# Optimization experiments

Measured on AMD Instinct MI355X. Metric: run time of the kernel, lower is better.

The kernel has to match this reference:

```python
import jax, jax.numpy as jnp
import numpy as np

PROBES = ["Fp1", "F3", "C3", "P3", "F7", "T3", "T5", "O1", "Fz", "Cz", "Pz",
          "Fp2", "F4", "C4", "P4", "F8", "T4", "T6", "O2"]
PROBE2IDX = {p: i for i, p in enumerate(PROBES)}
PROBE_GROUPS = {
    "LL": ["Fp1", "F7", "T3", "T5", "O1"],
    "LP": ["Fp1", "F3", "C3", "P3", "O1"],
    "RP": ["Fp2", "F8", "T4", "T6", "O2"],
    "RL": ["Fp2", "F4", "C4", "P4", "O2"],
    "Z": ["Fz", "Cz", "Pz"],
}
# Precompute bipolar-montage gather indices (18 derived channels)
_p1, _p2 = [], []
for _, probes in PROBE_GROUPS.items():
    for a, b in zip(probes[:-1], probes[1:]):
        _p1.append(PROBE2IDX[a]); _p2.append(PROBE2IDX[b])
I1 = np.asarray(_p1, dtype=np.int32)
I2 = np.asarray(_p2, dtype=np.int32)

FS = 200.0
FC_HP = 0.5
FC_LP = 50.0
Q = 0.7071067811865476  # torchaudio default Q = 1/sqrt(2)


def _biquad_coeffs(fs, fc, highpass):
    # torchaudio.functional.highpass_biquad / lowpass_biquad coefficients
    w0 = 2.0 * np.pi * fc / fs
    alpha = np.sin(w0) / (2.0 * Q)
    cw = np.cos(w0)
    a0 = 1.0 + alpha
    if highpass:
        b0 = (1.0 + cw) / 2.0
        b1 = -(1.0 + cw)
    else:
        b0 = (1.0 - cw) / 2.0
        b1 = 1.0 - cw
    b2 = b0
    a1 = -2.0 * cw
    a2 = 1.0 - alpha
    return (np.float32(b0 / a0), np.float32(b1 / a0), np.float32(b2 / a0),
            np.float32(a1 / a0), np.float32(a2 / a0))


def _biquad(x, coeffs):
    """Direct-form-I biquad along the last (time) axis. x: (B, C, T)."""
    b0, b1, b2, a1, a2 = coeffs

    def step(carry, xn):
        x1, x2, y1, y2 = carry
        y = b0 * xn + b1 * x1 + b2 * x2 - a1 * y1 - a2 * y2
        return (xn, x1, y, y1), y

    xt = jnp.moveaxis(x, -1, 0)  # (T, B, C)
    z = jnp.zeros_like(xt[0])
    _, yt = jax.lax.scan(step, (z, z, z, z), xt)
    return jnp.moveaxis(yt, 0, -1)  # (B, C, T)


def setup_inputs() -> dict:
    key = jax.random.key(0)
    k1, _ = jax.random.split(key)
    B, T, C = 64, 16384, 19
    x = jax.random.normal(k1, (B, T, C), dtype=jnp.float32)
    mask = jnp.ones((B, T, C), dtype=jnp.float32)
    return {"x": x, "mask": mask}


def reference(x, mask):
    # Bipolar montage: gather probe pairs and difference. (B, T, 18)
    d = x[..., I1] - x[..., I2]
    m = mask[..., I1] * mask[..., I2]
    eeg = jnp.swapaxes(d * m, 1, 2)       # apply_mask=True -> (B, 18, T)
    eeg_mask = jnp.swapaxes(m, 1, 2)      # (B, 18, T)
    # Cascaded biquad IIR: highpass(0.5 Hz) then lowpass(50 Hz)
    eeg = _biquad(eeg, _biquad_coeffs(FS, FC_HP, highpass=True))
    eeg = _biquad(eeg, _biquad_coeffs(FS, FC_LP, highpass=False))
    # clip_val is None -> no clamp
    return eeg, eeg_mask
```

## Files before the change

kernel.cpp:

```cpp
#include <hip/hip_runtime.h>
#include <cmath>

#define B_SZ 64
#define T_LEN 16384
#define NCH 18
#define NPROBE 19
#define TT 256
#define NTILE (T_LEN / TT)

typedef float nfloat4 __attribute__((ext_vector_type(4)));
typedef _Float16 half8 __attribute__((ext_vector_type(8)));

struct FiltConsts {
  float b0, b1, b2, a1, a2;
  float m[8][4];
};
struct BothFilt { FiltConsts f[2]; };

__device__ __forceinline__ int sw_idx(int idx) {
  return (idx & ~63) | ((idx + (idx >> 6)) & 63);
}

template <bool HALF_WS>
__global__ __launch_bounds__(256)
void montage_kernel(const float* __restrict__ x, const float* __restrict__ mask,
                    float* __restrict__ out, _Float16* __restrict__ wh) {
  __shared__ float buf[TT * NPROBE];
  const int tid = threadIdx.x;
  const int b = blockIdx.x >> 6;
  const int tile = blockIdx.x & 63;
  const int t0 = tile * TT;

  const size_t gbase = ((size_t)b * T_LEN + t0) * NPROBE;
  constexpr int N4 = TT * NPROBE / 4;

  const float4* xg = reinterpret_cast<const float4*>(x + gbase);
#pragma unroll
  for (int k = 0; k < 5; ++k) {
    int i = tid + k * 256;
    if (i < N4) reinterpret_cast<float4*>(buf)[i] = xg[i];
  }
  __syncthreads();
  float xv[NPROBE];
#pragma unroll
  for (int j = 0; j < NPROBE; ++j) xv[j] = buf[tid * NPROBE + j];
  __syncthreads();

  const float4* mg = reinterpret_cast<const float4*>(mask + gbase);
#pragma unroll
  for (int k = 0; k < 5; ++k) {
    int i = tid + k * 256;
    if (i < N4) reinterpret_cast<float4*>(buf)[i] = mg[i];
  }
  __syncthreads();
  float mv[NPROBE];
#pragma unroll
  for (int j = 0; j < NPROBE; ++j) mv[j] = buf[tid * NPROBE + j];

  const int I1[NCH] = {0,4,5,6, 0,1,2,3, 11,15,16,17, 11,12,13,14, 8,9};
  const int I2[NCH] = {4,5,6,7, 1,2,3,7, 15,16,17,18, 12,13,14,18, 9,10};
  const int t = t0 + tid;
  const size_t base = (size_t)b * NCH * T_LEN + t;
  const size_t half = (size_t)B_SZ * NCH * T_LEN;
#pragma unroll
  for (int ch = 0; ch < NCH; ++ch) {
    float d = xv[I1[ch]] - xv[I2[ch]];
    float m = mv[I1[ch]] * mv[I2[ch]];
    if (HALF_WS) {
      wh[base + (size_t)ch * T_LEN] = (_Float16)(d * m);
    } else {
      out[base + (size_t)ch * T_LEN] = d * m;
    }
    __builtin_nontemporal_store(m, &out[half + base + (size_t)ch * T_LEN]);
  }
}

template <bool HALF_WS>
__global__ __launch_bounds__(256)
void filter_kernel(float* __restrict__ out, const _Float16* __restrict__ wh,
                   BothFilt fc) {
  __shared__ float row[T_LEN];
  __shared__ float2 scanbuf[256];
  const int tid = threadIdx.x;
  float* rp = out + (size_t)blockIdx.x * T_LEN;

  if (HALF_WS) {
    const half8* hp = reinterpret_cast<const half8*>(wh + (size_t)blockIdx.x * T_LEN);
#pragma unroll
    for (int k = 0; k < 8; ++k) {
      int i8 = tid + k * 256;
      half8 v = hp[i8];
      int e = i8 * 8;
#pragma unroll
      for (int j = 0; j < 8; ++j) row[sw_idx(e + j)] = (float)v[j];
    }
  } else {
#pragma unroll
    for (int k = 0; k < 16; ++k) {
      int i4 = tid + k * 256;
      float4 v = reinterpret_cast<const float4*>(rp)[i4];
      int e = i4 * 4;
      row[sw_idx(e + 0)] = v.x; row[sw_idx(e + 1)] = v.y;
      row[sw_idx(e + 2)] = v.z; row[sw_idx(e + 3)] = v.w;
    }
  }
  __syncthreads();

  const int e0 = tid * 64;
#pragma unroll
  for (int f = 0; f < 2; ++f) {
    const FiltConsts& F = fc.f[f];
    const float b0 = F.b0, b1 = F.b1, b2 = F.b2;
    const float na1 = -F.a1, na2 = -F.a2;

    float x1 = 0.f, x2 = 0.f;
    if (tid > 0) { x1 = row[sw_idx(e0 - 1)]; x2 = row[sw_idx(e0 - 2)]; }
    __syncthreads();
    float y1 = 0.f, y2 = 0.f;
#pragma unroll 4
    for (int n = 0; n < 64; ++n) {
      int a = sw_idx(e0 + n);
      float xn = row[a];
      float acc = b0 * xn;
      acc = fmaf(b1, x1, acc);
      acc = fmaf(b2, x2, acc);
      acc = fmaf(na1, y1, acc);
      acc = fmaf(na2, y2, acc);
      row[a] = acc;
      x2 = x1; x1 = xn;
      y2 = y1; y1 = acc;
    }
    scanbuf[tid] = make_float2(y1, y2);
    __syncthreads();

#pragma unroll
    for (int k = 0; k < 8; ++k) {
      const int off = 1 << k;
      const bool act = (tid >= off);
      float2 prev, mine;
      if (act) { prev = scanbuf[tid - off]; mine = scanbuf[tid]; }
      __syncthreads();
      if (act) {
        scanbuf[tid] = make_float2(
            fmaf(F.m[k][0], prev.x, fmaf(F.m[k][1], prev.y, mine.x)),
            fmaf(F.m[k][2], prev.x, fmaf(F.m[k][3], prev.y, mine.y)));
      }
      __syncthreads();
    }

    if (tid > 0) {
      float2 s = scanbuf[tid - 1];
      float c1 = s.x, c2 = s.y;
#pragma unroll 4
      for (int n = 0; n < 64; ++n) {
        int a = sw_idx(e0 + n);
        float cn = fmaf(na1, c1, na2 * c2);
        row[a] += cn;
        c2 = c1; c1 = cn;
      }
    }
    __syncthreads();
  }

#pragma unroll
  for (int k = 0; k < 16; ++k) {
    int i4 = tid + k * 256;
    int e = i4 * 4;
    nfloat4 v = { row[sw_idx(e + 0)], row[sw_idx(e + 1)],
                  row[sw_idx(e + 2)], row[sw_idx(e + 3)] };
    __builtin_nontemporal_store(v, reinterpret_cast<nfloat4*>(rp) + i4);
  }
}

static inline void mat2mul(const double* A, const double* Bm, double* C) {
  double c0 = A[0]*Bm[0] + A[1]*Bm[2];
  double c1 = A[0]*Bm[1] + A[1]*Bm[3];
  double c2 = A[2]*Bm[0] + A[3]*Bm[2];
  double c3 = A[2]*Bm[1] + A[3]*Bm[3];
  C[0]=c0; C[1]=c1; C[2]=c2; C[3]=c3;
}

static void fill_filt(FiltConsts* F, double fc, bool hp) {
  const double Q = 0.7071067811865476;
  const double fs = 200.0;
  const double PI = 3.14159265358979323846;
  double w0 = 2.0 * PI * fc / fs;
  double alpha = std::sin(w0) / (2.0 * Q);
  double cw = std::cos(w0);
  double a0 = 1.0 + alpha;
  double b0, b1;
  if (hp) { b0 = (1.0 + cw) * 0.5; b1 = -(1.0 + cw); }
  else    { b0 = (1.0 - cw) * 0.5; b1 = (1.0 - cw); }
  double b2 = b0;
  double a1 = -2.0 * cw;
  double a2 = 1.0 - alpha;
  F->b0 = (float)(b0 / a0); F->b1 = (float)(b1 / a0); F->b2 = (float)(b2 / a0);
  F->a1 = (float)(a1 / a0); F->a2 = (float)(a2 / a0);
  double A[4] = { -(double)F->a1, -(double)F->a2, 1.0, 0.0 };
  double M[4] = { A[0], A[1], A[2], A[3] };
  for (int i = 0; i < 6; ++i) mat2mul(M, M, M);
  for (int k = 0; k < 8; ++k) {
    F->m[k][0] = (float)M[0]; F->m[k][1] = (float)M[1];
    F->m[k][2] = (float)M[2]; F->m[k][3] = (float)M[3];
    mat2mul(M, M, M);
  }
}

extern "C" void kernel_launch(void* const* d_in, const int* in_sizes, int n_in,
                              void* d_out, int out_size, void* d_ws, size_t ws_size,
                              hipStream_t stream) {
  const float* x    = (const float*)d_in[0];
  const float* mask = (const float*)d_in[1];
  float* out = (float*)d_out;
  _Float16* wh = (_Float16*)d_ws;

  BothFilt bf;
  fill_filt(&bf.f[0], 0.5, true);
  fill_filt(&bf.f[1], 50.0, false);

  const size_t ws_needed = (size_t)B_SZ * NCH * T_LEN * sizeof(_Float16);
  if (ws_size >= ws_needed) {
    hipLaunchKernelGGL((montage_kernel<true>), dim3(B_SZ * NTILE), dim3(256), 0, stream,
                       x, mask, out, wh);
    hipLaunchKernelGGL((filter_kernel<true>), dim3(B_SZ * NCH), dim3(256), 0, stream,
                       out, wh, bf);
  } else {
    hipLaunchKernelGGL((montage_kernel<false>), dim3(B_SZ * NTILE), dim3(256), 0, stream,
                       x, mask, out, wh);
    hipLaunchKernelGGL((filter_kernel<false>), dim3(B_SZ * NCH), dim3(256), 0, stream,
                       out, wh, bf);
  }
}
```

Before: 101.2 us.

## Restructure montage kernel into single-wave blocks with grid-stride tiles

```diff
diff --git a/kernel.cpp b/kernel.cpp
--- a/kernel.cpp
+++ b/kernel.cpp
@@ -5,8 +5,9 @@
 #define T_LEN 16384
 #define NCH 18
 #define NPROBE 19
-#define TT 256
-#define NTILE (T_LEN / TT)
+#define WT 64
+#define NTILES (B_SZ * (T_LEN / WT))
+#define MGRID 4096
 
 typedef float nfloat4 __attribute__((ext_vector_type(4)));
 typedef _Float16 half8 __attribute__((ext_vector_type(8)));
@@ -22,56 +23,56 @@
 }
 
 template <bool HALF_WS>
-__global__ __launch_bounds__(256)
+__global__ __launch_bounds__(64)
 void montage_kernel(const float* __restrict__ x, const float* __restrict__ mask,
                     float* __restrict__ out, _Float16* __restrict__ wh) {
-  __shared__ float buf[TT * NPROBE];
-  const int tid = threadIdx.x;
-  const int b = blockIdx.x >> 6;
-  const int tile = blockIdx.x & 63;
-  const int t0 = tile * TT;
-
-  const size_t gbase = ((size_t)b * T_LEN + t0) * NPROBE;
-  constexpr int N4 = TT * NPROBE / 4;
-
-  const float4* xg = reinterpret_cast<const float4*>(x + gbase);
-#pragma unroll
-  for (int k = 0; k < 5; ++k) {
-    int i = tid + k * 256;
-    if (i < N4) reinterpret_cast<float4*>(buf)[i] = xg[i];
-  }
-  __syncthreads();
-  float xv[NPROBE];
-#pragma unroll
-  for (int j = 0; j < NPROBE; ++j) xv[j] = buf[tid * NPROBE + j];
-  __syncthreads();
-
-  const float4* mg = reinterpret_cast<const float4*>(mask + gbase);
-#pragma unroll
-  for (int k = 0; k < 5; ++k) {
-    int i = tid + k * 256;
-    if (i < N4) reinterpret_cast<float4*>(buf)[i] = mg[i];
-  }
-  __syncthreads();
-  float mv[NPROBE];
-#pragma unroll
-  for (int j = 0; j < NPROBE; ++j) mv[j] = buf[tid * NPROBE + j];
-
+  __shared__ __align__(16) float lx[WT * NPROBE];
+  __shared__ __align__(16) float lm[WT * NPROBE];
+  const int lane = threadIdx.x;
   const int I1[NCH] = {0,4,5,6, 0,1,2,3, 11,15,16,17, 11,12,13,14, 8,9};
   const int I2[NCH] = {4,5,6,7, 1,2,3,7, 15,16,17,18, 12,13,14,18, 9,10};
-  const int t = t0 + tid;
-  const size_t base = (size_t)b * NCH * T_LEN + t;
   const size_t half = (size_t)B_SZ * NCH * T_LEN;
-#pragma unroll
-  for (int ch = 0; ch < NCH; ++ch) {
-    float d = xv[I1[ch]] - xv[I2[ch]];
-    float m = mv[I1[ch]] * mv[I2[ch]];
-    if (HALF_WS) {
-      wh[base + (size_t)ch * T_LEN] = (_Float16)(d * m);
-    } else {
-      out[base + (size_t)ch * T_LEN] = d * m;
-    }
-    __builtin_nontemporal_store(m, &out[half + base + (size_t)ch * T_LEN]);
+  constexpr int N4 = WT * NPROBE / 4;
+
+  for (int tile = blockIdx.x; tile < NTILES; tile += MGRID) {
+    const int b = tile >> 8;
+    const int seg = tile & 255;
+    const int t0 = seg * WT;
+
+    const size_t gbase = ((size_t)b * T_LEN + t0) * NPROBE;
+    const float4* xg = reinterpret_cast<const float4*>(x + gbase);
+    const float4* mg = reinterpret_cast<const float4*>(mask + gbase);
+#pragma unroll
+    for (int r = 0; r < 5; ++r) {
+      int i = lane + r * 64;
+      if (i < N4) {
+        reinterpret_cast<float4*>(lx)[i] = xg[i];
+        reinterpret_cast<float4*>(lm)[i] = mg[i];
+      }
+    }
+    __syncthreads();
+
+    float xv[NPROBE], mv[NPROBE];
+#pragma unroll
+    for (int j = 0; j < NPROBE; ++j) {
+      xv[j] = lx[lane * NPROBE + j];
+      mv[j] = lm[lane * NPROBE + j];
+    }
+
+    const int t = t0 + lane;
+    const size_t base = (size_t)b * NCH * T_LEN + t;
+#pragma unroll
+    for (int ch = 0; ch < NCH; ++ch) {
+      float d = xv[I1[ch]] - xv[I2[ch]];
+      float m = mv[I1[ch]] * mv[I2[ch]];
+      if (HALF_WS) {
+        wh[base + (size_t)ch * T_LEN] = (_Float16)(d * m);
+      } else {
+        out[base + (size_t)ch * T_LEN] = d * m;
+      }
+      __builtin_nontemporal_store(m, &out[half + base + (size_t)ch * T_LEN]);
+    }
+    __syncthreads();
   }
 }
 
@@ -220,12 +221,12 @@
 
   const size_t ws_needed = (size_t)B_SZ * NCH * T_LEN * sizeof(_Float16);
   if (ws_size >= ws_needed) {
-    hipLaunchKernelGGL((montage_kernel<true>), dim3(B_SZ * NTILE), dim3(256), 0, stream,
+    hipLaunchKernelGGL((montage_kernel<true>), dim3(MGRID), dim3(64), 0, stream,
                        x, mask, out, wh);
     hipLaunchKernelGGL((filter_kernel<true>), dim3(B_SZ * NCH), dim3(256), 0, stream,
                        out, wh, bf);
   } else {
-    hipLaunchKernelGGL((montage_kernel<false>), dim3(B_SZ * NTILE), dim3(256), 0, stream,
+    hipLaunchKernelGGL((montage_kernel<false>), dim3(MGRID), dim3(64), 0, stream,
                        x, mask, out, wh);
     hipLaunchKernelGGL((filter_kernel<false>), dim3(B_SZ * NCH), dim3(256), 0, stream,
                        out, wh, bf);
```

Measured after the change: 102.2 us. About the same (+1.0%).
